# Kernel tuning notes

Hardware: AMD Instinct MI355X
Metric: run time of the kernel (lower is better)

## Reference

```python
import jax, jax.numpy as jnp
import numpy as np

B, S, D, H = 2, 2048, 1024, 16
DK = D // H

def setup_inputs() -> dict:
    key = jax.random.key(0)
    k1, k2, k3 = jax.random.split(key, 3)
    std = 2.0 / (D + 3 * D)
    x = jax.random.normal(k1, (B, S, D), dtype=jnp.float32)
    W_qkv = jax.random.normal(k2, (3 * D, D), dtype=jnp.float32) * std
    W_out = jax.random.normal(k3, (D, D), dtype=jnp.float32) * (2.0 / (2 * D))
    return {"x": x, "W_qkv": W_qkv, "W_out": W_out}

def reference(x, W_qkv, W_out):
    # fused QKV projection: [..., d_in] x [d_out, d_in] -> [..., d_out]
    proj = jnp.einsum('bsd,ed->bse', x, W_qkv)               # [B,S,3*H*DK]
    proj = proj.reshape(B, S, 3, H, DK)
    q = proj[:, :, 0].transpose(0, 2, 1, 3)                  # [B,H,S,DK]
    k = proj[:, :, 1].transpose(0, 2, 1, 3)
    v = proj[:, :, 2].transpose(0, 2, 1, 3)
    scores = jnp.einsum('bhnd,bhmd->bhnm', q, k) / jnp.sqrt(jnp.float32(DK))
    causal = jnp.tril(jnp.ones((S, S), dtype=bool))
    scores = jnp.where(causal, scores, -jnp.inf)
    attn = jax.nn.softmax(scores, axis=-1)
    out = jnp.einsum('bhnm,bhmd->bhnd', attn, v)             # [B,H,S,DK]
    out = out.transpose(0, 2, 1, 3).reshape(B, S, H * DK)
    return jnp.einsum('bsd,ed->bse', out, W_out)             # [B,S,D]
```

## Files before the change

kernel.cpp:

```cpp
#include <hip/hip_runtime.h>
#include <hip/hip_bf16.h>
#include <stdint.h>

typedef __attribute__((ext_vector_type(8))) __bf16 bf16x8;
typedef __attribute__((ext_vector_type(8))) short  short8;
typedef __attribute__((ext_vector_type(4))) float  f32x4;

#define MFMA16(a, b, c) __builtin_amdgcn_mfma_f32_16x16x32_bf16((a), (b), (c), 0, 0, 0)

__device__ __forceinline__ unsigned short f32_bf16(float f) {
  union { float f; unsigned u; } v; v.f = f;
  unsigned r = v.u + 0x7FFFu + ((v.u >> 16) & 1u);
  return (unsigned short)(r >> 16);
}

__device__ __forceinline__ void gload16(const unsigned short* g, unsigned short* l) {
  __builtin_amdgcn_global_load_lds(
      (const __attribute__((address_space(1))) unsigned int*)(g),
      (__attribute__((address_space(3))) unsigned int*)(l), 16, 0, 0);
}

__global__ void cvt3_kernel(const float* __restrict__ a, int na4,
                            const float* __restrict__ b, int nb4,
                            const float* __restrict__ c, int nc4,
                            unsigned short* __restrict__ oa,
                            unsigned short* __restrict__ ob,
                            unsigned short* __restrict__ oc) {
  int total = na4 + nb4 + nc4;
  for (int i = blockIdx.x * blockDim.x + threadIdx.x; i < total; i += gridDim.x * blockDim.x) {
    const float* src; unsigned short* dst; int j = i;
    if (j < na4) { src = a; dst = oa; }
    else if (j - na4 < nb4) { j -= na4; src = b; dst = ob; }
    else { j -= na4 + nb4; src = c; dst = oc; }
    float4 v = reinterpret_cast<const float4*>(src)[j];
    ushort4 o4;
    o4.x = f32_bf16(v.x); o4.y = f32_bf16(v.y);
    o4.z = f32_bf16(v.z); o4.w = f32_bf16(v.w);
    reinterpret_cast<ushort4*>(dst)[j] = o4;
  }
}

template <int MODE>
__global__ __launch_bounds__(256) void gemm_bt(const unsigned short* __restrict__ A,
                                               const unsigned short* __restrict__ Bm,
                                               void* __restrict__ Cout,
                                               int M, int N, int K) {
  extern __shared__ unsigned short SM[];
  unsigned short* As = SM;
  unsigned short* Bs = SM + 4096;
  const int tid  = threadIdx.x;
  const int lane = tid & 63;
  const int wid  = tid >> 6;
  const int wr   = wid >> 1, wc = wid & 1;
  const int l16  = lane & 15, lh = lane >> 4;
  const int m0   = blockIdx.y * 128;
  const int n0   = blockIdx.x * 128;

  f32x4 acc[4][4];
#pragma unroll
  for (int mi = 0; mi < 4; ++mi)
#pragma unroll
    for (int ni = 0; ni < 4; ++ni) acc[mi][ni] = 0.f;

  const int c0 = tid, c1 = 256 + tid;
  const unsigned short* a0 = A + (size_t)(m0 + (c0 >> 2)) * K + (c0 & 3) * 8;
  const unsigned short* a1 = A + (size_t)(m0 + (c1 >> 2)) * K + (c1 & 3) * 8;
  const unsigned short* b0 = Bm + (size_t)(n0 + (c0 >> 2)) * K + (c0 & 3) * 8;
  const unsigned short* b1 = Bm + (size_t)(n0 + (c1 >> 2)) * K + (c1 & 3) * 8;
  const int d0 = wid * 64 * 8;
  const int d1 = (256 + wid * 64) * 8;

  for (int k0 = 0; k0 < K; k0 += 32) {
    __syncthreads();
    gload16(a0 + k0, As + d0);
    gload16(a1 + k0, As + d1);
    gload16(b0 + k0, Bs + d0);
    gload16(b1 + k0, Bs + d1);
    __syncthreads();
    bf16x8 af[4], bfr[4];
#pragma unroll
    for (int i = 0; i < 4; ++i) {
      af[i]  = *(const bf16x8*)(As + (wr * 64 + i * 16 + l16) * 32 + lh * 8);
      bfr[i] = *(const bf16x8*)(Bs + (wc * 64 + i * 16 + l16) * 32 + lh * 8);
    }
#pragma unroll
    for (int mi = 0; mi < 4; ++mi)
#pragma unroll
      for (int ni = 0; ni < 4; ++ni)
        acc[mi][ni] = MFMA16(af[mi], bfr[ni], acc[mi][ni]);
  }

  __syncthreads();
  unsigned short* Ep = SM + wid * 4096;

  if (MODE == 0) {
    const int gn0 = n0 + wc * 64;
    const int cc  = gn0 >> 10;
    const int hh2 = (gn0 & 1023) >> 6;
    const int gm0 = m0 + wr * 64;
    const int bb2 = gm0 >> 11;
    const int ss0 = gm0 & 2047;
    const int bh2 = bb2 * 16 + hh2;
    unsigned short* qkv = (unsigned short*)Cout;

    if (cc < 2) {
      const float qsc = (cc == 0) ? 0.18033688f : 1.0f;
#pragma unroll
      for (int mi = 0; mi < 4; ++mi)
#pragma unroll
        for (int ni = 0; ni < 4; ++ni)
#pragma unroll
          for (int r = 0; r < 4; ++r) {
            int row = mi * 16 + lh * 4 + r;
            int col = (ni * 16 + l16) ^ (lh << 3);
            Ep[row * 64 + col] = f32_bf16(acc[mi][ni][r] * qsc);
          }
      unsigned short* qk = qkv + (((size_t)cc * 32 + bh2) * 2048 + ss0) * 64;
#pragma unroll
      for (int it = 0; it < 8; ++it) {
        int ci = it * 64 + lane;
        int row = ci >> 3, c = ci & 7;
        short8 vv = *(const short8*)(Ep + row * 64 + ((c ^ ((row >> 2) & 3)) * 8));
        *(short8*)(qk + (size_t)row * 64 + c * 8) = vv;
      }
    } else {
#pragma unroll
      for (int mi = 0; mi < 4; ++mi)
#pragma unroll
        for (int ni = 0; ni < 4; ++ni) {
          int dk = ni * 16 + l16;
          int ssl = mi * 16 + lh * 4;
          unsigned lo, hi;
          asm("v_cvt_pk_bf16_f32 %0, %1, %2" : "=v"(lo) : "v"(acc[mi][ni][0]), "v"(acc[mi][ni][1]));
          asm("v_cvt_pk_bf16_f32 %0, %1, %2" : "=v"(hi) : "v"(acc[mi][ni][2]), "v"(acc[mi][ni][3]));
          int off = dk * 64 + (ssl ^ ((dk & 7) << 3));
          *(uint2*)(Ep + off) = make_uint2(lo, hi);
        }
      unsigned short* vt = qkv + (size_t)8388608 + (size_t)bh2 * 64 * 2048 + ss0;
#pragma unroll
      for (int it = 0; it < 8; ++it) {
        int ci = it * 64 + lane;
        int dk = ci >> 3, c = ci & 7;
        short8 vv = *(const short8*)(Ep + dk * 64 + ((c ^ (dk & 7)) * 8));
        *(short8*)(vt + (size_t)dk * 2048 + c * 8) = vv;
      }
    }
  } else {
    float* C = (float*)Cout;
    float* Ef = (float*)Ep;
    const int gm0 = m0 + wr * 64;
    const int gn0 = n0 + wc * 64;
#pragma unroll
    for (int p = 0; p < 2; ++p) {
#pragma unroll
      for (int mi = 0; mi < 4; ++mi)
#pragma unroll
        for (int q = 0; q < 2; ++q) {
          int ni = 2 * p + q;
#pragma unroll
          for (int r = 0; r < 4; ++r) {
            int row = mi * 16 + lh * 4 + r;
            int col = (q * 16 + l16) ^ ((row & 7) << 2);
            Ef[row * 32 + col] = acc[mi][ni][r];
          }
        }
#pragma unroll
      for (int it = 0; it < 8; ++it) {
        int ci = it * 64 + lane;
        int row = ci >> 3, c4 = ci & 7;
        float4 vv = *(const float4*)(Ef + row * 32 + ((c4 * 4) ^ ((row & 7) << 2)));
        *(float4*)(&C[(size_t)(gm0 + row) * N + gn0 + p * 32 + c4 * 4]) = vv;
      }
    }
  }
}

__global__ __launch_bounds__(256) void attn_kernel(const unsigned short* __restrict__ Qg,
                                                   const unsigned short* __restrict__ Kg,
                                                   const unsigned short* __restrict__ Vtg,
                                                   unsigned short* __restrict__ Og) {
  __shared__ unsigned short Ks[2][64 * 64];
  __shared__ unsigned short Vs[2][64 * 64];
  __shared__ unsigned short Pl[4][16 * 64];

  const int tid  = threadIdx.x;
  const int lane = tid & 63;
  const int w    = tid >> 6;
  const int l16  = lane & 15, lh = lane >> 4;
  const int j    = blockIdx.x >> 5;
  const int ring = j >> 3, k = j & 7;
  const int qt   = (ring == 0) ? 31 - k : (ring == 1) ? k : (ring == 2) ? 23 - k : 8 + k;
  const int bh   = blockIdx.x & 31;
  const int bb   = bh >> 4, hh = bh & 15;
  const int qb   = qt * 64;
  const int wqb  = qb + w * 16;

  const unsigned short* Qh = Qg + (size_t)bh * (2048 * 64);
  const unsigned short* Kh = Kg + (size_t)bh * (2048 * 64);
  const unsigned short* Vh = Vtg + (size_t)bh * (64 * 2048);

  bf16x8 qf[2];
#pragma unroll
  for (int h2 = 0; h2 < 2; ++h2)
    qf[h2] = *(const bf16x8*)(Qh + (size_t)(wqb + l16) * 64 + h2 * 32 + lh * 8);

  float mreg = 0.f;
  float ll   = 0.f;
  f32x4 o[4];
#pragma unroll
  for (int f = 0; f < 4; ++f) o[f] = 0.f;

  const int sA = tid, sB = tid + 256;
  const int rA = sA >> 3, hA = (sA & 7) ^ (rA & 7);
  const int rB = sB >> 3, hB = (sB & 7) ^ (rB & 7);
  const unsigned short* kSrcA = Kh + rA * 64 + hA * 8;
  const unsigned short* kSrcB = Kh + rB * 64 + hB * 8;
  const unsigned short* vSrcA = Vh + (size_t)rA * 2048 + hA * 8;
  const unsigned short* vSrcB = Vh + (size_t)rB * 2048 + hB * 8;
  const int ldsA = w * 64 * 8;
  const int ldsB = (256 + w * 64) * 8;

  const int sw = l16 & 7;
  const int ntiles = qt + 1;

  gload16(kSrcA, &Ks[0][ldsA]);
  gload16(kSrcB, &Ks[0][ldsB]);
  gload16(vSrcA, &Vs[0][ldsA]);
  gload16(vSrcB, &Vs[0][ldsB]);
  __syncthreads();

  for (int t = 0; t < ntiles; ++t) {
    const int kv0 = t * 64;
    const int cur = t & 1;
    if (t + 1 < ntiles) {
      const int nk = kv0 + 64;
      gload16(kSrcA + (size_t)nk * 64, &Ks[cur ^ 1][ldsA]);
      gload16(kSrcB + (size_t)nk * 64, &Ks[cur ^ 1][ldsB]);
      gload16(vSrcA + nk, &Vs[cur ^ 1][ldsA]);
      gload16(vSrcB + nk, &Vs[cur ^ 1][ldsB]);
    }

    {
      const unsigned short* Kb = Ks[cur];
      const unsigned short* Vb = Vs[cur];
      __builtin_amdgcn_s_setprio(1);

      f32x4 st[4];
#pragma unroll
      for (int tt = 0; tt < 4; ++tt) {
        const unsigned short* krow = Kb + (tt * 16 + l16) * 64;
        bf16x8 kf0 = *(const bf16x8*)(krow + ((lh ^ sw) * 8));
        bf16x8 kf1 = *(const bf16x8*)(krow + (((lh + 4) ^ sw) * 8));
        f32x4 a = {0.f, 0.f, 0.f, 0.f};
        a = MFMA16(kf0, qf[0], a);
        a = MFMA16(kf1, qf[1], a);
        st[tt] = a;
      }

      if (kv0 + 63 > wqb) {
        int qrow = wqb + l16;
#pragma unroll
        for (int tt = 0; tt < 4; ++tt) {
          int kvb = kv0 + tt * 16 + lh * 4;
#pragma unroll
          for (int r = 0; r < 4; ++r)
            if (kvb + r > qrow) st[tt][r] = -__builtin_inff();
        }
      }

      float pm = fmaxf(fmaxf(st[0][0], st[0][1]), fmaxf(st[0][2], st[0][3]));
#pragma unroll
      for (int tt = 1; tt < 4; ++tt)
        pm = fmaxf(pm, fmaxf(fmaxf(st[tt][0], st[tt][1]), fmaxf(st[tt][2], st[tt][3])));
      if (!__all(pm <= mreg + 8.f)) {
        float t0 = pm;
        t0 = fmaxf(t0, __shfl_xor(t0, 16));
        t0 = fmaxf(t0, __shfl_xor(t0, 32));
        float mn = fmaxf(mreg, t0);
        float er = exp2f(mreg - mn);
        mreg = mn;
        ll *= er;
#pragma unroll
        for (int r = 0; r < 4; ++r) {
          float e = __shfl(er, lh * 4 + r);
#pragma unroll
          for (int f = 0; f < 4; ++f) o[f][r] *= e;
        }
      }

      unsigned short* Pw = Pl[w];
      int rbase = l16 * 64;
      float ps = 0.f;
#pragma unroll
      for (int tt = 0; tt < 4; ++tt) {
        float p0 = exp2f(st[tt][0] - mreg);
        float p1 = exp2f(st[tt][1] - mreg);
        float p2 = exp2f(st[tt][2] - mreg);
        float p3 = exp2f(st[tt][3] - mreg);
        ps += (p0 + p1) + (p2 + p3);
        unsigned lo, hi;
        asm("v_cvt_pk_bf16_f32 %0, %1, %2" : "=v"(lo) : "v"(p0), "v"(p1));
        asm("v_cvt_pk_bf16_f32 %0, %1, %2" : "=v"(hi) : "v"(p2), "v"(p3));
        int c8 = tt * 2 + (lh >> 1);
        int off = rbase + ((c8 ^ sw) << 3) + (lh & 1) * 4;
        *(uint2*)(Pw + off) = make_uint2(lo, hi);
      }
      float rs = ps;
      rs += __shfl_xor(rs, 16);
      rs += __shfl_xor(rs, 32);
      ll += rs;

      bf16x8 pf0 = *(const bf16x8*)(Pw + rbase + ((lh ^ sw) * 8));
      bf16x8 pf1 = *(const bf16x8*)(Pw + rbase + (((lh + 4) ^ sw) * 8));
#pragma unroll
      for (int f = 0; f < 4; ++f) {
        const unsigned short* vrow = Vb + (f * 16 + l16) * 64;
        bf16x8 vf0 = *(const bf16x8*)(vrow + ((lh ^ sw) * 8));
        bf16x8 vf1 = *(const bf16x8*)(vrow + (((lh + 4) ^ sw) * 8));
        o[f] = MFMA16(pf0, vf0, o[f]);
        o[f] = MFMA16(pf1, vf1, o[f]);
      }
      __builtin_amdgcn_s_setprio(0);
    }
    __syncthreads();
  }

  unsigned short* op = Og + (size_t)bb * 2048 * 1024 + (size_t)hh * 64;
#pragma unroll
  for (int r = 0; r < 4; ++r) {
    float linv = 1.f / __shfl(ll, lh * 4 + r);
    int row = wqb + lh * 4 + r;
#pragma unroll
    for (int f = 0; f < 4; ++f)
      op[(size_t)row * 1024 + f * 16 + l16] = f32_bf16(o[f][r] * linv);
  }
}

extern "C" void kernel_launch(void* const* d_in, const int* in_sizes, int n_in,
                              void* d_out, int out_size, void* d_ws, size_t ws_size,
                              hipStream_t stream) {
  const float* x    = (const float*)d_in[0];
  const float* Wqkv = (const float*)d_in[1];
  const float* Wout = (const float*)d_in[2];
  float* out = (float*)d_out;

  char* ws = (char*)d_ws;
  unsigned short* xb  = (unsigned short*)(ws);
  unsigned short* wqb = (unsigned short*)(ws + (size_t)8 * 1024 * 1024);
  unsigned short* wob = (unsigned short*)(ws + (size_t)14 * 1024 * 1024);
  unsigned short* qkv = (unsigned short*)(ws + (size_t)16 * 1024 * 1024);
  unsigned short* att = (unsigned short*)(ws + (size_t)40 * 1024 * 1024);

  cvt3_kernel<<<2048, 256, 0, stream>>>(x, 4194304 / 4, Wqkv, 3145728 / 4,
                                        Wout, 1048576 / 4, xb, wqb, wob);

  gemm_bt<0><<<dim3(24, 32), 256, 32768, stream>>>(xb, wqb, (void*)qkv, 4096, 3072, 1024);

  const unsigned short* Qp  = qkv;
  const unsigned short* Kp  = qkv + 4194304;
  const unsigned short* Vtp = qkv + 8388608;
  attn_kernel<<<1024, 256, 0, stream>>>(Qp, Kp, Vtp, att);

  gemm_bt<1><<<dim3(8, 32), 256, 32768, stream>>>(att, wob, (void*)out, 4096, 1024, 1024);
}
```

Measured before the change: 125.9 us.

## Replace QKV projection GEMM with 256x256-tile, 8-wave, phase-pipelined kernel

The QKV projection moves from a 128x128, 4-wave GEMM with K-step 32 to a dedicated 256x256, 8-wave kernel with K-step 64. It uses 128KB of double-buffered, XOR-swizzled LDS and interleaves async global-to-LDS loads with four MFMA phases separated by barriers and priority hints. The goal is more data reuse per tile and load latency hidden behind MFMA work. The costs are only 192 blocks, which may underfill the CUs, heavy LDS use that limits occupancy, and more barriers per iteration.

```diff
diff --git a/kernel.cpp b/kernel.cpp
--- a/kernel.cpp
+++ b/kernel.cpp
@@ -40,11 +40,167 @@
   }
 }
 
-template <int MODE>
-__global__ __launch_bounds__(256) void gemm_bt(const unsigned short* __restrict__ A,
-                                               const unsigned short* __restrict__ Bm,
-                                               void* __restrict__ Cout,
-                                               int M, int N, int K) {
+__global__ __launch_bounds__(512, 2) void gemm_qkv_8ph(const unsigned short* __restrict__ A,
+                                                       const unsigned short* __restrict__ Bm,
+                                                       unsigned short* __restrict__ qkv) {
+  extern __shared__ unsigned short SM[];
+  const int tid  = threadIdx.x;
+  const int lane = tid & 63;
+  const int w    = tid >> 6;
+  const int wr   = w >> 2, wc = w & 3;
+  const int l16  = lane & 15, lh = lane >> 4;
+  const int sw   = l16 & 7;
+  const int m0   = blockIdx.y * 256;
+  const int n0   = blockIdx.x * 256;
+
+  f32x4 acc[8][4];
+#pragma unroll
+  for (int mi = 0; mi < 8; ++mi)
+#pragma unroll
+    for (int ni = 0; ni < 4; ++ni) acc[mi][ni] = 0.f;
+
+  const int r0 = tid >> 3,         h0 = (tid & 7) ^ (r0 & 7);
+  const int r1 = (tid + 512) >> 3, h1 = (tid & 7) ^ (r1 & 7);
+  const unsigned short* Asrc[2][2];
+  const unsigned short* Bsrc[2][2];
+  Asrc[0][0] = A + (size_t)(m0 + r0) * 1024 + h0 * 8;
+  Asrc[0][1] = A + (size_t)(m0 + r1) * 1024 + h1 * 8;
+  Asrc[1][0] = A + (size_t)(m0 + 128 + r0) * 1024 + h0 * 8;
+  Asrc[1][1] = A + (size_t)(m0 + 128 + r1) * 1024 + h1 * 8;
+  Bsrc[0][0] = Bm + (size_t)(n0 + r0) * 1024 + h0 * 8;
+  Bsrc[0][1] = Bm + (size_t)(n0 + r1) * 1024 + h1 * 8;
+  Bsrc[1][0] = Bm + (size_t)(n0 + 128 + r0) * 1024 + h0 * 8;
+  Bsrc[1][1] = Bm + (size_t)(n0 + 128 + r1) * 1024 + h1 * 8;
+  const int ld0 = (w * 64) * 8;
+  const int ld1 = (512 + w * 64) * 8;
+
+#define STAGE_A(buf, h, U) do { \
+    gload16(Asrc[h][0] + (U) * 64, SM + (buf) * 32768 + (h) * 8192 + ld0); \
+    gload16(Asrc[h][1] + (U) * 64, SM + (buf) * 32768 + (h) * 8192 + ld1); } while (0)
+#define STAGE_B(buf, h, U) do { \
+    gload16(Bsrc[h][0] + (U) * 64, SM + (buf) * 32768 + 16384 + (h) * 8192 + ld0); \
+    gload16(Bsrc[h][1] + (U) * 64, SM + (buf) * 32768 + 16384 + (h) * 8192 + ld1); } while (0)
+
+  STAGE_A(0, 0, 0); STAGE_A(0, 1, 0);
+  STAGE_B(0, 0, 0); STAGE_B(0, 1, 0);
+  STAGE_B(1, 0, 1); STAGE_B(1, 1, 1);
+  asm volatile("s_waitcnt vmcnt(4)" ::: "memory");
+  __builtin_amdgcn_s_barrier();
+
+  const int NT = 16;
+#pragma unroll 2
+  for (int U = 0; U < NT; ++U) {
+    const int b = U & 1;
+    const unsigned short* Ab = SM + b * 32768 + wr * 8192;
+    const unsigned short* Bb = SM + b * 32768 + 16384 + (wc >> 1) * 8192;
+    const int rB = (wc & 1) * 64;
+    bf16x8 bfr[4][2], af[2][2];
+
+#define LDA(i, j) (*(const bf16x8*)(Ab + (((i) * 16 + l16) * 8 + (((j) * 4 + lh) ^ sw)) * 8))
+#define LDB(n, j) (*(const bf16x8*)(Bb + (((rB + (n) * 16 + l16)) * 8 + (((j) * 4 + lh) ^ sw)) * 8))
+#define PHASE_MFMA(p) \
+    __builtin_amdgcn_s_setprio(1); \
+    _Pragma("unroll") \
+    for (int n = 0; n < 4; ++n) { \
+      acc[2*(p)][n]   = MFMA16(af[0][0], bfr[n][0], acc[2*(p)][n]); \
+      acc[2*(p)][n]   = MFMA16(af[0][1], bfr[n][1], acc[2*(p)][n]); \
+      acc[2*(p)+1][n] = MFMA16(af[1][0], bfr[n][0], acc[2*(p)+1][n]); \
+      acc[2*(p)+1][n] = MFMA16(af[1][1], bfr[n][1], acc[2*(p)+1][n]); \
+    } \
+    __builtin_amdgcn_s_setprio(0);
+
+    af[0][0] = LDA(0, 0); af[0][1] = LDA(0, 1);
+    af[1][0] = LDA(1, 0); af[1][1] = LDA(1, 1);
+#pragma unroll
+    for (int n = 0; n < 4; ++n) { bfr[n][0] = LDB(n, 0); bfr[n][1] = LDB(n, 1); }
+    if (U + 1 < NT) STAGE_A(b ^ 1, 0, U + 1);
+    __builtin_amdgcn_s_barrier();
+    PHASE_MFMA(0)
+    __builtin_amdgcn_s_barrier();
+    af[0][0] = LDA(2, 0); af[0][1] = LDA(2, 1);
+    af[1][0] = LDA(3, 0); af[1][1] = LDA(3, 1);
+    if (U + 1 < NT) STAGE_A(b ^ 1, 1, U + 1);
+    __builtin_amdgcn_s_barrier();
+    PHASE_MFMA(1)
+    __builtin_amdgcn_s_barrier();
+    af[0][0] = LDA(4, 0); af[0][1] = LDA(4, 1);
+    af[1][0] = LDA(5, 0); af[1][1] = LDA(5, 1);
+    if (U + 2 < NT) STAGE_B(b, 0, U + 2);
+    __builtin_amdgcn_s_barrier();
+    PHASE_MFMA(2)
+    __builtin_amdgcn_s_barrier();
+    af[0][0] = LDA(6, 0); af[0][1] = LDA(6, 1);
+    af[1][0] = LDA(7, 0); af[1][1] = LDA(7, 1);
+    if (U + 2 < NT) STAGE_B(b, 1, U + 2);
+    __builtin_amdgcn_s_barrier();
+    PHASE_MFMA(3)
+    asm volatile("s_waitcnt vmcnt(4)" ::: "memory");
+    __builtin_amdgcn_s_barrier();
+#undef LDA
+#undef LDB
+#undef PHASE_MFMA
+  }
+
+  __syncthreads();
+  unsigned short* Ep = SM + w * 8192;
+  const int gn0 = n0 + wc * 64;
+  const int cc  = gn0 >> 10;
+  const int hh2 = (gn0 & 1023) >> 6;
+  const int gm0 = m0 + wr * 128;
+  const int bb2 = gm0 >> 11;
+  const int ss0 = gm0 & 2047;
+  const int bh2 = bb2 * 16 + hh2;
+
+  if (cc < 2) {
+    const float qsc = (cc == 0) ? 0.18033688f : 1.0f;
+#pragma unroll
+    for (int mi = 0; mi < 8; ++mi)
+#pragma unroll
+      for (int ni = 0; ni < 4; ++ni)
+#pragma unroll
+        for (int r = 0; r < 4; ++r) {
+          int row = mi * 16 + lh * 4 + r;
+          int col = (ni * 16 + l16) ^ (lh << 3);
+          Ep[row * 64 + col] = f32_bf16(acc[mi][ni][r] * qsc);
+        }
+    unsigned short* qk = qkv + (((size_t)cc * 32 + bh2) * 2048 + ss0) * 64;
+#pragma unroll
+    for (int it = 0; it < 16; ++it) {
+      int ci = it * 64 + lane;
+      int row = ci >> 3, c = ci & 7;
+      short8 vv = *(const short8*)(Ep + row * 64 + ((c ^ ((row >> 2) & 3)) * 8));
+      *(short8*)(qk + (size_t)row * 64 + c * 8) = vv;
+    }
+  } else {
+#pragma unroll
+    for (int mi = 0; mi < 8; ++mi)
+#pragma unroll
+      for (int ni = 0; ni < 4; ++ni) {
+        int dk = ni * 16 + l16;
+        int ssl = mi * 16 + lh * 4;
+        unsigned lo, hi;
+        asm("v_cvt_pk_bf16_f32 %0, %1, %2" : "=v"(lo) : "v"(acc[mi][ni][0]), "v"(acc[mi][ni][1]));
+        asm("v_cvt_pk_bf16_f32 %0, %1, %2" : "=v"(hi) : "v"(acc[mi][ni][2]), "v"(acc[mi][ni][3]));
+        int off = dk * 128 + (ssl ^ ((dk & 7) << 3));
+        *(uint2*)(Ep + off) = make_uint2(lo, hi);
+      }
+    unsigned short* vt = qkv + (size_t)8388608 + (size_t)bh2 * 64 * 2048 + ss0;
+#pragma unroll
+    for (int it = 0; it < 16; ++it) {
+      int ci = it * 64 + lane;
+      int dk = ci >> 4, c = ci & 15;
+      short8 vv = *(const short8*)(Ep + dk * 128 + ((c ^ (dk & 7)) * 8));
+      *(short8*)(vt + (size_t)dk * 2048 + c * 8) = vv;
+    }
+  }
+#undef STAGE_A
+#undef STAGE_B
+}
+
+__global__ __launch_bounds__(256) void gemm_out(const unsigned short* __restrict__ A,
+                                                const unsigned short* __restrict__ Bm,
+                                                float* __restrict__ C,
+                                                int M, int N, int K) {
   extern __shared__ unsigned short SM[];
   unsigned short* As = SM;
   unsigned short* Bs = SM + 4096;
@@ -91,86 +247,29 @@
   }
 
   __syncthreads();
-  unsigned short* Ep = SM + wid * 4096;
-
-  if (MODE == 0) {
-    const int gn0 = n0 + wc * 64;
-    const int cc  = gn0 >> 10;
-    const int hh2 = (gn0 & 1023) >> 6;
-    const int gm0 = m0 + wr * 64;
-    const int bb2 = gm0 >> 11;
-    const int ss0 = gm0 & 2047;
-    const int bh2 = bb2 * 16 + hh2;
-    unsigned short* qkv = (unsigned short*)Cout;
-
-    if (cc < 2) {
-      const float qsc = (cc == 0) ? 0.18033688f : 1.0f;
-#pragma unroll
-      for (int mi = 0; mi < 4; ++mi)
-#pragma unroll
-        for (int ni = 0; ni < 4; ++ni)
-#pragma unroll
-          for (int r = 0; r < 4; ++r) {
-            int row = mi * 16 + lh * 4 + r;
-            int col = (ni * 16 + l16) ^ (lh << 3);
-            Ep[row * 64 + col] = f32_bf16(acc[mi][ni][r] * qsc);
-          }
-      unsigned short* qk = qkv + (((size_t)cc * 32 + bh2) * 2048 + ss0) * 64;
-#pragma unroll
-      for (int it = 0; it < 8; ++it) {
-        int ci = it * 64 + lane;
-        int row = ci >> 3, c = ci & 7;
-        short8 vv = *(const short8*)(Ep + row * 64 + ((c ^ ((row >> 2) & 3)) * 8));
-        *(short8*)(qk + (size_t)row * 64 + c * 8) = vv;
-      }
-    } else {
-#pragma unroll
-      for (int mi = 0; mi < 4; ++mi)
-#pragma unroll
-        for (int ni = 0; ni < 4; ++ni) {
-          int dk = ni * 16 + l16;
-          int ssl = mi * 16 + lh * 4;
-          unsigned lo, hi;
-          asm("v_cvt_pk_bf16_f32 %0, %1, %2" : "=v"(lo) : "v"(acc[mi][ni][0]), "v"(acc[mi][ni][1]));
-          asm("v_cvt_pk_bf16_f32 %0, %1, %2" : "=v"(hi) : "v"(acc[mi][ni][2]), "v"(acc[mi][ni][3]));
-          int off = dk * 64 + (ssl ^ ((dk & 7) << 3));
-          *(uint2*)(Ep + off) = make_uint2(lo, hi);
+  float* Ef = (float*)(SM + wid * 4096);
+  const int gm0 = m0 + wr * 64;
+  const int gn0 = n0 + wc * 64;
+#pragma unroll
+  for (int p = 0; p < 2; ++p) {
+#pragma unroll
+    for (int mi = 0; mi < 4; ++mi)
+#pragma unroll
+      for (int q = 0; q < 2; ++q) {
+        int ni = 2 * p + q;
+#pragma unroll
+        for (int r = 0; r < 4; ++r) {
+          int row = mi * 16 + lh * 4 + r;
+          int col = (q * 16 + l16) ^ ((row & 7) << 2);
+          Ef[row * 32 + col] = acc[mi][ni][r];
         }
-      unsigned short* vt = qkv + (size_t)8388608 + (size_t)bh2 * 64 * 2048 + ss0;
-#pragma unroll
-      for (int it = 0; it < 8; ++it) {
-        int ci = it * 64 + lane;
-        int dk = ci >> 3, c = ci & 7;
-        short8 vv = *(const short8*)(Ep + dk * 64 + ((c ^ (dk & 7)) * 8));
-        *(short8*)(vt + (size_t)dk * 2048 + c * 8) = vv;
-      }
-    }
-  } else {
-    float* C = (float*)Cout;
-    float* Ef = (float*)Ep;
-    const int gm0 = m0 + wr * 64;
-    const int gn0 = n0 + wc * 64;
-#pragma unroll
-    for (int p = 0; p < 2; ++p) {
-#pragma unroll
-      for (int mi = 0; mi < 4; ++mi)
-#pragma unroll
-        for (int q = 0; q < 2; ++q) {
-          int ni = 2 * p + q;
-#pragma unroll
-          for (int r = 0; r < 4; ++r) {
-            int row = mi * 16 + lh * 4 + r;
-            int col = (q * 16 + l16) ^ ((row & 7) << 2);
-            Ef[row * 32 + col] = acc[mi][ni][r];
-          }
-        }
-#pragma unroll
-      for (int it = 0; it < 8; ++it) {
-        int ci = it * 64 + lane;
-        int row = ci >> 3, c4 = ci & 7;
-        float4 vv = *(const float4*)(Ef + row * 32 + ((c4 * 4) ^ ((row & 7) << 2)));
-        *(float4*)(&C[(size_t)(gm0 + row) * N + gn0 + p * 32 + c4 * 4]) = vv;
-      }
+      }
+#pragma unroll
+    for (int it = 0; it < 8; ++it) {
+      int ci = it * 64 + lane;
+      int row = ci >> 3, c4 = ci & 7;
+      float4 vv = *(const float4*)(Ef + row * 32 + ((c4 * 4) ^ ((row & 7) << 2)));
+      *(float4*)(&C[(size_t)(gm0 + row) * N + gn0 + p * 32 + c4 * 4]) = vv;
     }
   }
 }
@@ -351,15 +450,22 @@
   unsigned short* qkv = (unsigned short*)(ws + (size_t)16 * 1024 * 1024);
   unsigned short* att = (unsigned short*)(ws + (size_t)40 * 1024 * 1024);
 
+  static bool attr_set = false;
+  if (!attr_set) {
+    hipFuncSetAttribute((const void*)gemm_qkv_8ph,
+                        hipFuncAttributeMaxDynamicSharedMemorySize, 131072);
+    attr_set = true;
+  }
+
   cvt3_kernel<<<2048, 256, 0, stream>>>(x, 4194304 / 4, Wqkv, 3145728 / 4,
                                         Wout, 1048576 / 4, xb, wqb, wob);
 
-  gemm_bt<0><<<dim3(24, 32), 256, 32768, stream>>>(xb, wqb, (void*)qkv, 4096, 3072, 1024);
+  gemm_qkv_8ph<<<dim3(12, 16), 512, 131072, stream>>>(xb, wqb, qkv);
 
   const unsigned short* Qp  = qkv;
   const unsigned short* Kp  = qkv + 4194304;
   const unsigned short* Vtp = qkv + 8388608;
   attn_kernel<<<1024, 256, 0, stream>>>(Qp, Kp, Vtp, att);
 
-  gemm_bt<1><<<dim3(8, 32), 256, 32768, stream>>>(att, wob, (void*)out, 4096, 1024, 1024);
-}
+  gemm_out<<<dim3(8, 32), 256, 32768, stream>>>(att, wob, out, 4096, 1024, 1024);
+}
```

New measurement: 118.0 us. -6.3%, faster.
